# Kernel optimization log

Hardware: AMD Instinct MI355X
Metric: run time of the kernel (lower is better)

The kernel has to match this reference:

```python
import jax, jax.numpy as jnp
import numpy as np

D = 1024      # total input features
R = 32        # number of ragged regions
RMAX = 32     # max region size (padding target)
HIDDEN = [128, 128]
H1, H2 = HIDDEN
B = 8192      # batch size


def _made_masks(r, rmax, hidden):
    """TFP AutoregressiveNetwork masks (left-to-right order, 'equal' hidden degrees,
    params=2, use_bias=False), zero-padded to rmax features."""
    order = np.arange(1, r + 1)
    degs = [order]
    for u in hidden:
        mn = min(int(degs[-1].min()), r - 1)
        degs.append(np.maximum(mn, np.ceil(np.arange(1, u + 1) * (r - 1) / float(u + 1)).astype(np.int64)))
    m1 = np.zeros((rmax, hidden[0]), bool)
    m1[:r] = degs[0][:, None] <= degs[1][None, :]
    m2 = degs[1][:, None] <= degs[2][None, :]
    mout = np.zeros((hidden[-1], rmax * 2), bool)
    out_deg = np.repeat(order, 2)  # output layout is feature-major: [feat, param]
    mout[:, :2 * r] = degs[-1][:, None] < out_deg[None, :]
    return m1, m2, mout


def setup_inputs() -> dict:
    rng = np.random.default_rng(0)
    perm = rng.permutation(D)
    sizes = rng.integers(8, RMAX + 1, size=R)
    idx = np.zeros((R, RMAX), np.int64)
    valid = np.zeros((R, RMAX), bool)
    M1 = np.zeros((R, RMAX, H1), bool)
    M2 = np.zeros((R, H1, H2), bool)
    Mout = np.zeros((R, H2, RMAX * 2), bool)
    pos = 0
    for i in range(R):
        s = int(sizes[i])
        idx[i, :s] = perm[pos:pos + s]
        pos += s
        valid[i, :s] = True
        M1[i], M2[i], Mout[i] = _made_masks(s, RMAX, HIDDEN)
    key = jax.random.key(0)
    k1, k2, k3, k4 = jax.random.split(key, 4)
    inputs = jax.random.normal(k1, (B, D), jnp.float32)
    W1 = jax.random.normal(k2, (R, RMAX, H1), jnp.float32) / np.float32(np.sqrt(RMAX))
    W2 = jax.random.normal(k3, (R, H1, H2), jnp.float32) / np.float32(np.sqrt(H1))
    Wout = jax.random.normal(k4, (R, H2, RMAX * 2), jnp.float32) / np.float32(np.sqrt(H2))
    return {"inputs": inputs, "W1": W1, "W2": W2, "Wout": Wout,
            "idx": jnp.asarray(idx), "valid": jnp.asarray(valid),
            "M1": jnp.asarray(M1), "M2": jnp.asarray(M2), "Mout": jnp.asarray(Mout)}


def reference(inputs, W1, W2, Wout, idx, valid, M1, M2, Mout):
    f = inputs.dtype
    v = valid.astype(f)                              # [R, RMAX]
    xg = jnp.take(inputs, idx, axis=1) * v           # [B, R, RMAX] ragged gather (padded)
    # MADE masked MLP (relu, no bias), batched over all regions at once
    h1 = jax.nn.relu(jnp.einsum('brd,rdh->brh', xg, W1 * M1.astype(f)))
    h2 = jax.nn.relu(jnp.einsum('brh,rhk->brk', h1, W2 * M2.astype(f)))
    out = jnp.einsum('brk,rko->bro', h2, Wout * Mout.astype(f))
    out = out.reshape(out.shape[0], out.shape[1], RMAX, 2)
    shift, log_s = out[..., 0], out[..., 1]
    # MAF inverse: u = (x - shift) * exp(-log_scale); logdet = -sum(log_scale)
    u = (xg - shift) * jnp.exp(-log_s)
    elem = -0.5 * u * u - 0.5 * jnp.log(2.0 * jnp.pi) - log_s
    ll = jnp.sum(elem * v, axis=-1)                  # [B, R]
    return ll[..., None]                             # [B, R, 1] as in tf.stack of expand_dims
```

## Files before the change

### kernel.cpp

```cpp
#include <hip/hip_runtime.h>
#include <math.h>


#define RR 32
#define DD 1024
#define HH 128
#define OO 64
#define TROWS 32
#define TILES_PER_BLOCK 16
#define BLOCKS_PER_R 16

#define SHP 136
#define SXG 40
#define SXF 38
#define SSC 132

typedef short bf16x8_t __attribute__((ext_vector_type(8)));
typedef float f32x4_t __attribute__((ext_vector_type(4)));
typedef unsigned short u16;
typedef unsigned int u32;

__device__ __forceinline__ u16 bf16_rne(float x) {
    u32 u = __float_as_uint(x);
    u += 0x7FFFu + ((u >> 16) & 1u);
    return (u16)(u >> 16);
}
__device__ __forceinline__ float bf16_tof(u16 h) {
    return __uint_as_float(((u32)h) << 16);
}
__device__ __forceinline__ u16 lo_trunc(float v, u16 h) {
    return (u16)(__float_as_uint(v - bf16_tof(h)) >> 16);
}
__device__ __forceinline__ u32 pack_split(float v) {
    u16 h = bf16_rne(v);
    return (u32)h | ((u32)lo_trunc(v, h) << 16);
}
__device__ __forceinline__ void unpack8(const u32* p, bf16x8_t& hi, bf16x8_t& lo) {
    uint4 a = *reinterpret_cast<const uint4*>(p);
    uint4 b = *reinterpret_cast<const uint4*>(p + 4);
    union { u32 u[4]; bf16x8_t v; } H, L;
    H.u[0] = __builtin_amdgcn_perm(a.y, a.x, 0x05040100u);
    H.u[1] = __builtin_amdgcn_perm(a.w, a.z, 0x05040100u);
    H.u[2] = __builtin_amdgcn_perm(b.y, b.x, 0x05040100u);
    H.u[3] = __builtin_amdgcn_perm(b.w, b.z, 0x05040100u);
    L.u[0] = __builtin_amdgcn_perm(a.y, a.x, 0x07060302u);
    L.u[1] = __builtin_amdgcn_perm(a.w, a.z, 0x07060302u);
    L.u[2] = __builtin_amdgcn_perm(b.y, b.x, 0x07060302u);
    L.u[3] = __builtin_amdgcn_perm(b.w, b.z, 0x07060302u);
    hi = H.v; lo = L.v;
}
__device__ __forceinline__ f32x4_t mfma16(bf16x8_t a, bf16x8_t b, f32x4_t c) {
    return __builtin_amdgcn_mfma_f32_16x16x32_bf16(a, b, c, 0, 0, 0);
}

__device__ __forceinline__ void stage_block(const float* __restrict__ W,
                                            const int* __restrict__ M,
                                            int ldc, int c0, int K, u32* dst, int sd,
                                            int tid)
{
    const int kb = tid >> 3;
    const int cb = tid & 7;
    if (kb * 4 >= K) return;
    const int k0 = kb * 4;
    float e[4][4];
#pragma unroll
    for (int i = 0; i < 4; ++i) {
        const int o = ((k0 + i) * ldc + c0 + 4 * cb) >> 2;
        float4 w = ((const float4*)W)[o];
        int4   m = ((const int4*)M)[o];
        e[i][0] = m.x ? w.x : 0.f; e[i][1] = m.y ? w.y : 0.f;
        e[i][2] = m.z ? w.z : 0.f; e[i][3] = m.w ? w.w : 0.f;
    }
#pragma unroll
    for (int j = 0; j < 4; ++j) {
        uint4 p;
        p.x = pack_split(e[0][j]); p.y = pack_split(e[1][j]);
        p.z = pack_split(e[2][j]); p.w = pack_split(e[3][j]);
        *(uint4*)&dst[(4 * cb + j) * sd + k0] = p;
    }
}

__global__ __launch_bounds__(256, 2)
void made_flow_r9(const float* __restrict__ inputs,
                  const float* __restrict__ W1,
                  const float* __restrict__ W2,
                  const float* __restrict__ Wout,
                  const int* __restrict__ idx,
                  const int* __restrict__ valid,
                  const int* __restrict__ M1,
                  const int* __restrict__ M2,
                  const int* __restrict__ Mout,
                  float* __restrict__ out)
{
    __shared__ __align__(16) char regA[TROWS * SHP * 2 * 2];
    __shared__ __align__(16) char regB[TROWS * SHP * 2 * 2];
    __shared__ __align__(16) u16  xgh[2][TROWS * SXG];
    __shared__ __align__(16) u16  xgl[2][TROWS * SXG];
    __shared__ __align__(16) float xgf[2][TROWS * SXF];
    __shared__ __align__(16) float red_all[TILES_PER_BLOCK][TROWS][4];
    __shared__ int   idx_s[RR];
    __shared__ float v_s[RR];

    u16* const h1h = (u16*)regA;
    u16* const h1l = h1h + TROWS * SHP;
    u32* const scr = (u32*)regA;
    u16* const h2h = (u16*)regB;
    u16* const h2l = h2h + TROWS * SHP;

    const int tid  = threadIdx.x;
    const int r    = blockIdx.x / BLOCKS_PER_R;
    const int rb   = blockIdx.x % BLOCKS_PER_R;
    const int lane = tid & 63;
    const int wave = tid >> 6;
    const int q    = lane >> 4;
    const int l16  = lane & 15;

    if (tid < RR) {
        idx_s[tid] = idx[r * RR + tid];
        v_s[tid]   = valid[r * RR + tid] ? 1.f : 0.f;
    }

    bf16x8_t a1h[2], a1l[2];
    bf16x8_t a2h[2][4], a2l[2][4];
    bf16x8_t aoh[4],    aol[4];
    {
        const float* W1r = W1 + r * RR * HH;   const int* M1r = M1 + r * RR * HH;
        const float* W2r = W2 + r * HH * HH;   const int* M2r = M2 + r * HH * HH;
        const float* Wor = Wout + r * HH * OO; const int* Mor = Mout + r * HH * OO;
        for (int c = 0; c < 4; ++c) {
            __syncthreads();
            stage_block(W2r, M2r, HH, 32 * c, HH, scr, SSC, tid);
            __syncthreads();
            if (wave == c) {
#pragma unroll
                for (int mi = 0; mi < 2; ++mi)
#pragma unroll
                    for (int ks = 0; ks < 4; ++ks)
                        unpack8(&scr[(16 * mi + l16) * SSC + ks * 32 + q * 8],
                                a2h[mi][ks], a2l[mi][ks]);
            }
        }
        for (int c = 0; c < 2; ++c) {
            __syncthreads();
            stage_block(Wor, Mor, OO, 32 * c, HH, scr, SSC, tid);
            __syncthreads();
            if ((wave >> 1) == c) {
                const int nl = wave & 1;
#pragma unroll
                for (int ks = 0; ks < 4; ++ks)
                    unpack8(&scr[(16 * nl + l16) * SSC + ks * 32 + q * 8],
                            aoh[ks], aol[ks]);
            }
        }
        for (int c = 0; c < 4; ++c) {
            __syncthreads();
            stage_block(W1r, M1r, HH, 32 * c, RR, scr, SSC, tid);
            __syncthreads();
            if (wave == c) {
#pragma unroll
                for (int mi = 0; mi < 2; ++mi)
                    unpack8(&scr[(16 * mi + l16) * SSC + q * 8], a1h[mi], a1l[mi]);
            }
        }
    }
    __syncthreads();

    const f32x4_t zero4 = {0.f, 0.f, 0.f, 0.f};
    const int grow = tid >> 3, gg = tid & 7;

    {
        const int base = (rb * TILES_PER_BLOCK * TROWS + grow) * DD;
        float gx[4];
#pragma unroll
        for (int u = 0; u < 4; ++u)
            gx[u] = inputs[base + idx_s[4 * gg + u]] * v_s[4 * gg + u];
        ushort4 gh, gl;
        gh.x = bf16_rne(gx[0]); gl.x = lo_trunc(gx[0], gh.x);
        gh.y = bf16_rne(gx[1]); gl.y = lo_trunc(gx[1], gh.y);
        gh.z = bf16_rne(gx[2]); gl.z = lo_trunc(gx[2], gh.z);
        gh.w = bf16_rne(gx[3]); gl.w = lo_trunc(gx[3], gh.w);
        *(ushort4*)&xgh[0][grow * SXG + 4 * gg] = gh;
        *(ushort4*)&xgl[0][grow * SXG + 4 * gg] = gl;
        *(float2*)&xgf[0][grow * SXF + 4 * gg]     = make_float2(gx[0], gx[1]);
        *(float2*)&xgf[0][grow * SXF + 4 * gg + 2] = make_float2(gx[2], gx[3]);
    }
    __syncthreads();

    {
        bf16x8_t bh[2], bl[2];
#pragma unroll
        for (int ni = 0; ni < 2; ++ni) {
            bh[ni] = *(const bf16x8_t*)&xgh[0][(16 * ni + l16) * SXG + q * 8];
            bl[ni] = *(const bf16x8_t*)&xgl[0][(16 * ni + l16) * SXG + q * 8];
        }
#pragma unroll
        for (int mi = 0; mi < 2; ++mi)
#pragma unroll
            for (int ni = 0; ni < 2; ++ni) {
                f32x4_t a = zero4;
                a = mfma16(a1h[mi], bh[ni], a);
                a = mfma16(a1l[mi], bh[ni], a);
                a = mfma16(a1h[mi], bl[ni], a);
                ushort4 vh, vl;
                float v0 = fmaxf(a[0], 0.f), v1 = fmaxf(a[1], 0.f);
                float v2 = fmaxf(a[2], 0.f), v3 = fmaxf(a[3], 0.f);
                vh.x = bf16_rne(v0); vl.x = lo_trunc(v0, vh.x);
                vh.y = bf16_rne(v1); vl.y = lo_trunc(v1, vh.y);
                vh.z = bf16_rne(v2); vl.z = lo_trunc(v2, vh.z);
                vh.w = bf16_rne(v3); vl.w = lo_trunc(v3, vh.w);
                const int o = (16 * ni + l16) * SHP + 32 * wave + 16 * mi + 4 * q;
                *(ushort4*)&h1h[o] = vh;
                *(ushort4*)&h1l[o] = vl;
            }
    }

    for (int t = 0; t < TILES_PER_BLOCK; ++t) {
        const int row0 = (rb * TILES_PER_BLOCK + t) * TROWS;
        __syncthreads();

        float gx[4];
        const bool dg = (t + 1 < TILES_PER_BLOCK);
        if (dg) {
            const int base = (row0 + TROWS + grow) * DD;
#pragma unroll
            for (int u = 0; u < 4; ++u)
                gx[u] = inputs[base + idx_s[4 * gg + u]] * v_s[4 * gg + u];
        }
        {
            f32x4_t acc[2][2] = {{zero4, zero4}, {zero4, zero4}};
#pragma unroll
            for (int ks = 0; ks < 4; ++ks) {
#pragma unroll
                for (int ni = 0; ni < 2; ++ni) {
                    bf16x8_t bh = *(const bf16x8_t*)&h1h[(16 * ni + l16) * SHP + ks * 32 + q * 8];
                    bf16x8_t bl = *(const bf16x8_t*)&h1l[(16 * ni + l16) * SHP + ks * 32 + q * 8];
#pragma unroll
                    for (int mi = 0; mi < 2; ++mi) {
                        f32x4_t a = acc[mi][ni];
                        a = mfma16(a2h[mi][ks], bh, a);
                        a = mfma16(a2l[mi][ks], bh, a);
                        a = mfma16(a2h[mi][ks], bl, a);
                        acc[mi][ni] = a;
                    }
                }
            }
            if (dg) {
                const int b = (t + 1) & 1;
                ushort4 gh, gl;
                gh.x = bf16_rne(gx[0]); gl.x = lo_trunc(gx[0], gh.x);
                gh.y = bf16_rne(gx[1]); gl.y = lo_trunc(gx[1], gh.y);
                gh.z = bf16_rne(gx[2]); gl.z = lo_trunc(gx[2], gh.z);
                gh.w = bf16_rne(gx[3]); gl.w = lo_trunc(gx[3], gh.w);
                *(ushort4*)&xgh[b][grow * SXG + 4 * gg] = gh;
                *(ushort4*)&xgl[b][grow * SXG + 4 * gg] = gl;
                *(float2*)&xgf[b][grow * SXF + 4 * gg]     = make_float2(gx[0], gx[1]);
                *(float2*)&xgf[b][grow * SXF + 4 * gg + 2] = make_float2(gx[2], gx[3]);
            }
#pragma unroll
            for (int mi = 0; mi < 2; ++mi)
#pragma unroll
                for (int ni = 0; ni < 2; ++ni) {
                    ushort4 vh, vl;
                    float v0 = fmaxf(acc[mi][ni][0], 0.f), v1 = fmaxf(acc[mi][ni][1], 0.f);
                    float v2 = fmaxf(acc[mi][ni][2], 0.f), v3 = fmaxf(acc[mi][ni][3], 0.f);
                    vh.x = bf16_rne(v0); vl.x = lo_trunc(v0, vh.x);
                    vh.y = bf16_rne(v1); vl.y = lo_trunc(v1, vh.y);
                    vh.z = bf16_rne(v2); vl.z = lo_trunc(v2, vh.z);
                    vh.w = bf16_rne(v3); vl.w = lo_trunc(v3, vh.w);
                    const int o = (16 * ni + l16) * SHP + 32 * wave + 16 * mi + 4 * q;
                    *(ushort4*)&h2h[o] = vh;
                    *(ushort4*)&h2l[o] = vl;
                }
        }
        __syncthreads();

        f32x4_t acc3[2] = {zero4, zero4};
#pragma unroll
        for (int ks = 0; ks < 4; ++ks) {
#pragma unroll
            for (int ni = 0; ni < 2; ++ni) {
                bf16x8_t bh = *(const bf16x8_t*)&h2h[(16 * ni + l16) * SHP + ks * 32 + q * 8];
                bf16x8_t bl = *(const bf16x8_t*)&h2l[(16 * ni + l16) * SHP + ks * 32 + q * 8];
                f32x4_t a = acc3[ni];
                a = mfma16(aoh[ks], bh, a);
                a = mfma16(aol[ks], bh, a);
                a = mfma16(aoh[ks], bl, a);
                acc3[ni] = a;
            }
        }

        if (dg) {
            const int b = (t + 1) & 1;
            bf16x8_t bh[2], bl[2];
#pragma unroll
            for (int ni = 0; ni < 2; ++ni) {
                bh[ni] = *(const bf16x8_t*)&xgh[b][(16 * ni + l16) * SXG + q * 8];
                bl[ni] = *(const bf16x8_t*)&xgl[b][(16 * ni + l16) * SXG + q * 8];
            }
#pragma unroll
            for (int mi = 0; mi < 2; ++mi)
#pragma unroll
                for (int ni = 0; ni < 2; ++ni) {
                    f32x4_t a = zero4;
                    a = mfma16(a1h[mi], bh[ni], a);
                    a = mfma16(a1l[mi], bh[ni], a);
                    a = mfma16(a1h[mi], bl[ni], a);
                    ushort4 vh, vl;
                    float v0 = fmaxf(a[0], 0.f), v1 = fmaxf(a[1], 0.f);
                    float v2 = fmaxf(a[2], 0.f), v3 = fmaxf(a[3], 0.f);
                    vh.x = bf16_rne(v0); vl.x = lo_trunc(v0, vh.x);
                    vh.y = bf16_rne(v1); vl.y = lo_trunc(v1, vh.y);
                    vh.z = bf16_rne(v2); vl.z = lo_trunc(v2, vh.z);
                    vh.w = bf16_rne(v3); vl.w = lo_trunc(v3, vh.w);
                    const int o = (16 * ni + l16) * SHP + 32 * wave + 16 * mi + 4 * q;
                    *(ushort4*)&h1h[o] = vh;
                    *(ushort4*)&h1l[o] = vl;
                }
        }

        {
            const int j0 = 8 * wave + 2 * q;
            const float vj0 = v_s[j0], vj1 = v_s[j0 + 1];
            float p[2];
#pragma unroll
            for (int ni = 0; ni < 2; ++ni) {
                const int row = 16 * ni + l16;
                float2 xv = *(const float2*)&xgf[t & 1][row * SXF + j0];
                const float u0 = (xv.x - acc3[ni][0]) * __expf(-acc3[ni][1]);
                const float u1 = (xv.y - acc3[ni][2]) * __expf(-acc3[ni][3]);
                p[ni] = (-0.5f * u0 * u0 - 0.91893853320467266954f - acc3[ni][1]) * vj0
                      + (-0.5f * u1 * u1 - 0.91893853320467266954f - acc3[ni][3]) * vj1;
            }
#pragma unroll
            for (int ni = 0; ni < 2; ++ni) {
                p[ni] += __shfl_xor(p[ni], 16, 64);
                p[ni] += __shfl_xor(p[ni], 32, 64);
            }
            if (q == 0) {
#pragma unroll
                for (int ni = 0; ni < 2; ++ni)
                    red_all[t][16 * ni + l16][wave] = p[ni];
            }
        }
    }

    __syncthreads();
#pragma unroll
    for (int rep = 0; rep < 2; ++rep) {
        const int f   = tid + rep * 256;
        const int tt  = f >> 5;
        const int row = f & 31;
        float4 rv = *(const float4*)&red_all[tt][row][0];
        out[((rb * TILES_PER_BLOCK + tt) * TROWS + row) * RR + r] =
            rv.x + rv.y + rv.z + rv.w;
    }
}

extern "C" void kernel_launch(void* const* d_in, const int* in_sizes, int n_in,
                              void* d_out, int out_size, void* d_ws, size_t ws_size,
                              hipStream_t stream)
{
    const float* inputs = (const float*)d_in[0];
    const float* W1     = (const float*)d_in[1];
    const float* W2     = (const float*)d_in[2];
    const float* Wout   = (const float*)d_in[3];
    const int*   idx    = (const int*)d_in[4];
    const int*   valid  = (const int*)d_in[5];
    const int*   M1     = (const int*)d_in[6];
    const int*   M2     = (const int*)d_in[7];
    const int*   Mout   = (const int*)d_in[8];
    float*       out    = (float*)d_out;

    hipLaunchKernelGGL(made_flow_r9, dim3(RR * BLOCKS_PER_R), dim3(256), 0, stream,
                       inputs, W1, W2, Wout, idx, valid, M1, M2, Mout, out);
}
```

Before: 142.3 us.

## Double wavefronts per block, splitting MFMA tiles across eight waves

Raises the block from 256 to 512 threads. Each of the eight waves now holds half the register-resident weight fragments for W1, W2 and Wout and computes half the MFMA tiles per batch tile. Weight staging uses two scratch regions in parallel, one per half of the block, and the gather loads two elements per thread instead of four. The goal is more waves in flight to hide latency and less register pressure per wave. The cost is more threads contending at each barrier and a tighter launch bound of 4 blocks per unit.

```diff
diff --git a/kernel.cpp b/kernel.cpp
--- a/kernel.cpp
+++ b/kernel.cpp
@@ -80,17 +80,31 @@
     }
 }
 
-__global__ __launch_bounds__(256, 2)
-void made_flow_r9(const float* __restrict__ inputs,
-                  const float* __restrict__ W1,
-                  const float* __restrict__ W2,
-                  const float* __restrict__ Wout,
-                  const int* __restrict__ idx,
-                  const int* __restrict__ valid,
-                  const int* __restrict__ M1,
-                  const int* __restrict__ M2,
-                  const int* __restrict__ Mout,
-                  float* __restrict__ out)
+__device__ __forceinline__ void relu_pack_store(u16* __restrict__ h, u16* __restrict__ l,
+                                                int o, f32x4_t a)
+{
+    float v0 = fmaxf(a[0], 0.f), v1 = fmaxf(a[1], 0.f);
+    float v2 = fmaxf(a[2], 0.f), v3 = fmaxf(a[3], 0.f);
+    ushort4 vh, vl;
+    vh.x = bf16_rne(v0); vl.x = lo_trunc(v0, vh.x);
+    vh.y = bf16_rne(v1); vl.y = lo_trunc(v1, vh.y);
+    vh.z = bf16_rne(v2); vl.z = lo_trunc(v2, vh.z);
+    vh.w = bf16_rne(v3); vl.w = lo_trunc(v3, vh.w);
+    *(ushort4*)&h[o] = vh;
+    *(ushort4*)&l[o] = vl;
+}
+
+__global__ __launch_bounds__(512, 4)
+void made_flow_r10(const float* __restrict__ inputs,
+                   const float* __restrict__ W1,
+                   const float* __restrict__ W2,
+                   const float* __restrict__ Wout,
+                   const int* __restrict__ idx,
+                   const int* __restrict__ valid,
+                   const int* __restrict__ M1,
+                   const int* __restrict__ M2,
+                   const int* __restrict__ Mout,
+                   float* __restrict__ out)
 {
     __shared__ __align__(16) char regA[TROWS * SHP * 2 * 2];
     __shared__ __align__(16) char regB[TROWS * SHP * 2 * 2];
@@ -103,7 +117,8 @@
 
     u16* const h1h = (u16*)regA;
     u16* const h1l = h1h + TROWS * SHP;
-    u32* const scr = (u32*)regA;
+    u32* const scr  = (u32*)regA;
+    u32* const scr2 = (u32*)regB;
     u16* const h2h = (u16*)regB;
     u16* const h2l = h2h + TROWS * SHP;
 
@@ -114,75 +129,72 @@
     const int wave = tid >> 6;
     const int q    = lane >> 4;
     const int l16  = lane & 15;
+    const int wm3  = wave & 3;
+    const int ni3  = wave >> 2;
 
     if (tid < RR) {
         idx_s[tid] = idx[r * RR + tid];
         v_s[tid]   = valid[r * RR + tid] ? 1.f : 0.f;
     }
 
-    bf16x8_t a1h[2], a1l[2];
-    bf16x8_t a2h[2][4], a2l[2][4];
-    bf16x8_t aoh[4],    aol[4];
+    bf16x8_t a1h, a1l;
+    bf16x8_t a2h[4], a2l[4];
+    bf16x8_t aoh[4], aol[4];
     {
         const float* W1r = W1 + r * RR * HH;   const int* M1r = M1 + r * RR * HH;
         const float* W2r = W2 + r * HH * HH;   const int* M2r = M2 + r * HH * HH;
         const float* Wor = Wout + r * HH * OO; const int* Mor = Mout + r * HH * OO;
-        for (int c = 0; c < 4; ++c) {
-            __syncthreads();
-            stage_block(W2r, M2r, HH, 32 * c, HH, scr, SSC, tid);
-            __syncthreads();
-            if (wave == c) {
-#pragma unroll
-                for (int mi = 0; mi < 2; ++mi)
-#pragma unroll
-                    for (int ks = 0; ks < 4; ++ks)
-                        unpack8(&scr[(16 * mi + l16) * SSC + ks * 32 + q * 8],
-                                a2h[mi][ks], a2l[mi][ks]);
-            }
-        }
-        for (int c = 0; c < 2; ++c) {
-            __syncthreads();
-            stage_block(Wor, Mor, OO, 32 * c, HH, scr, SSC, tid);
-            __syncthreads();
-            if ((wave >> 1) == c) {
-                const int nl = wave & 1;
+        const int c = wave >> 1, h = wave & 1;
+        for (int i = 0; i < 2; ++i) {
+            __syncthreads();
+            if (tid < 256) stage_block(W2r, M2r, HH, 32 * (2 * i),     HH, scr,  SSC, tid);
+            else           stage_block(W2r, M2r, HH, 32 * (2 * i + 1), HH, scr2, SSC, tid - 256);
+            __syncthreads();
+            if (c == 2 * i) {
 #pragma unroll
                 for (int ks = 0; ks < 4; ++ks)
-                    unpack8(&scr[(16 * nl + l16) * SSC + ks * 32 + q * 8],
-                            aoh[ks], aol[ks]);
-            }
-        }
-        for (int c = 0; c < 4; ++c) {
-            __syncthreads();
-            stage_block(W1r, M1r, HH, 32 * c, RR, scr, SSC, tid);
-            __syncthreads();
-            if (wave == c) {
-#pragma unroll
-                for (int mi = 0; mi < 2; ++mi)
-                    unpack8(&scr[(16 * mi + l16) * SSC + q * 8], a1h[mi], a1l[mi]);
-            }
+                    unpack8(&scr[(16 * h + l16) * SSC + ks * 32 + q * 8], a2h[ks], a2l[ks]);
+            } else if (c == 2 * i + 1) {
+#pragma unroll
+                for (int ks = 0; ks < 4; ++ks)
+                    unpack8(&scr2[(16 * h + l16) * SSC + ks * 32 + q * 8], a2h[ks], a2l[ks]);
+            }
+        }
+        {
+            __syncthreads();
+            if (tid < 256) stage_block(Wor, Mor, OO, 0,  HH, scr,  SSC, tid);
+            else           stage_block(Wor, Mor, OO, 32, HH, scr2, SSC, tid - 256);
+            __syncthreads();
+            const u32* s = (wm3 >> 1) ? scr2 : scr;
+#pragma unroll
+            for (int ks = 0; ks < 4; ++ks)
+                unpack8(&s[(16 * (wm3 & 1) + l16) * SSC + ks * 32 + q * 8], aoh[ks], aol[ks]);
+        }
+        for (int i = 0; i < 2; ++i) {
+            __syncthreads();
+            if (tid < 256) stage_block(W1r, M1r, HH, 32 * (2 * i),     RR, scr,  SSC, tid);
+            else           stage_block(W1r, M1r, HH, 32 * (2 * i + 1), RR, scr2, SSC, tid - 256);
+            __syncthreads();
+            if (c == 2 * i)          unpack8(&scr [(16 * h + l16) * SSC + q * 8], a1h, a1l);
+            else if (c == 2 * i + 1) unpack8(&scr2[(16 * h + l16) * SSC + q * 8], a1h, a1l);
         }
     }
     __syncthreads();
 
     const f32x4_t zero4 = {0.f, 0.f, 0.f, 0.f};
-    const int grow = tid >> 3, gg = tid & 7;
+    const int grow = tid >> 4;
+    const int gg   = tid & 15;
 
     {
         const int base = (rb * TILES_PER_BLOCK * TROWS + grow) * DD;
-        float gx[4];
-#pragma unroll
-        for (int u = 0; u < 4; ++u)
-            gx[u] = inputs[base + idx_s[4 * gg + u]] * v_s[4 * gg + u];
-        ushort4 gh, gl;
-        gh.x = bf16_rne(gx[0]); gl.x = lo_trunc(gx[0], gh.x);
-        gh.y = bf16_rne(gx[1]); gl.y = lo_trunc(gx[1], gh.y);
-        gh.z = bf16_rne(gx[2]); gl.z = lo_trunc(gx[2], gh.z);
-        gh.w = bf16_rne(gx[3]); gl.w = lo_trunc(gx[3], gh.w);
-        *(ushort4*)&xgh[0][grow * SXG + 4 * gg] = gh;
-        *(ushort4*)&xgl[0][grow * SXG + 4 * gg] = gl;
-        *(float2*)&xgf[0][grow * SXF + 4 * gg]     = make_float2(gx[0], gx[1]);
-        *(float2*)&xgf[0][grow * SXF + 4 * gg + 2] = make_float2(gx[2], gx[3]);
+        float gx0 = inputs[base + idx_s[2 * gg]]     * v_s[2 * gg];
+        float gx1 = inputs[base + idx_s[2 * gg + 1]] * v_s[2 * gg + 1];
+        ushort2 gh, gl;
+        gh.x = bf16_rne(gx0); gl.x = lo_trunc(gx0, gh.x);
+        gh.y = bf16_rne(gx1); gl.y = lo_trunc(gx1, gh.y);
+        *(ushort2*)&xgh[0][grow * SXG + 2 * gg] = gh;
+        *(ushort2*)&xgl[0][grow * SXG + 2 * gg] = gl;
+        *(float2*)&xgf[0][grow * SXF + 2 * gg] = make_float2(gx0, gx1);
     }
     __syncthreads();
 
@@ -194,99 +206,64 @@
             bl[ni] = *(const bf16x8_t*)&xgl[0][(16 * ni + l16) * SXG + q * 8];
         }
 #pragma unroll
-        for (int mi = 0; mi < 2; ++mi)
-#pragma unroll
-            for (int ni = 0; ni < 2; ++ni) {
-                f32x4_t a = zero4;
-                a = mfma16(a1h[mi], bh[ni], a);
-                a = mfma16(a1l[mi], bh[ni], a);
-                a = mfma16(a1h[mi], bl[ni], a);
-                ushort4 vh, vl;
-                float v0 = fmaxf(a[0], 0.f), v1 = fmaxf(a[1], 0.f);
-                float v2 = fmaxf(a[2], 0.f), v3 = fmaxf(a[3], 0.f);
-                vh.x = bf16_rne(v0); vl.x = lo_trunc(v0, vh.x);
-                vh.y = bf16_rne(v1); vl.y = lo_trunc(v1, vh.y);
-                vh.z = bf16_rne(v2); vl.z = lo_trunc(v2, vh.z);
-                vh.w = bf16_rne(v3); vl.w = lo_trunc(v3, vh.w);
-                const int o = (16 * ni + l16) * SHP + 32 * wave + 16 * mi + 4 * q;
-                *(ushort4*)&h1h[o] = vh;
-                *(ushort4*)&h1l[o] = vl;
-            }
+        for (int ni = 0; ni < 2; ++ni) {
+            f32x4_t a = zero4;
+            a = mfma16(a1h, bh[ni], a);
+            a = mfma16(a1l, bh[ni], a);
+            a = mfma16(a1h, bl[ni], a);
+            relu_pack_store(h1h, h1l, (16 * ni + l16) * SHP + 16 * wave + 4 * q, a);
+        }
     }
 
     for (int t = 0; t < TILES_PER_BLOCK; ++t) {
         const int row0 = (rb * TILES_PER_BLOCK + t) * TROWS;
         __syncthreads();
 
-        float gx[4];
+        float gx0, gx1;
         const bool dg = (t + 1 < TILES_PER_BLOCK);
         if (dg) {
             const int base = (row0 + TROWS + grow) * DD;
-#pragma unroll
-            for (int u = 0; u < 4; ++u)
-                gx[u] = inputs[base + idx_s[4 * gg + u]] * v_s[4 * gg + u];
+            gx0 = inputs[base + idx_s[2 * gg]]     * v_s[2 * gg];
+            gx1 = inputs[base + idx_s[2 * gg + 1]] * v_s[2 * gg + 1];
         }
         {
-            f32x4_t acc[2][2] = {{zero4, zero4}, {zero4, zero4}};
+            f32x4_t acc[2] = {zero4, zero4};
 #pragma unroll
             for (int ks = 0; ks < 4; ++ks) {
 #pragma unroll
                 for (int ni = 0; ni < 2; ++ni) {
                     bf16x8_t bh = *(const bf16x8_t*)&h1h[(16 * ni + l16) * SHP + ks * 32 + q * 8];
                     bf16x8_t bl = *(const bf16x8_t*)&h1l[(16 * ni + l16) * SHP + ks * 32 + q * 8];
-#pragma unroll
-                    for (int mi = 0; mi < 2; ++mi) {
-                        f32x4_t a = acc[mi][ni];
-                        a = mfma16(a2h[mi][ks], bh, a);
-                        a = mfma16(a2l[mi][ks], bh, a);
-                        a = mfma16(a2h[mi][ks], bl, a);
-                        acc[mi][ni] = a;
-                    }
+                    f32x4_t a = acc[ni];
+                    a = mfma16(a2h[ks], bh, a);
+                    a = mfma16(a2l[ks], bh, a);
+                    a = mfma16(a2h[ks], bl, a);
+                    acc[ni] = a;
                 }
             }
             if (dg) {
                 const int b = (t + 1) & 1;
-                ushort4 gh, gl;
-                gh.x = bf16_rne(gx[0]); gl.x = lo_trunc(gx[0], gh.x);
-                gh.y = bf16_rne(gx[1]); gl.y = lo_trunc(gx[1], gh.y);
-                gh.z = bf16_rne(gx[2]); gl.z = lo_trunc(gx[2], gh.z);
-                gh.w = bf16_rne(gx[3]); gl.w = lo_trunc(gx[3], gh.w);
-                *(ushort4*)&xgh[b][grow * SXG + 4 * gg] = gh;
-                *(ushort4*)&xgl[b][grow * SXG + 4 * gg] = gl;
-                *(float2*)&xgf[b][grow * SXF + 4 * gg]     = make_float2(gx[0], gx[1]);
-                *(float2*)&xgf[b][grow * SXF + 4 * gg + 2] = make_float2(gx[2], gx[3]);
-            }
-#pragma unroll
-            for (int mi = 0; mi < 2; ++mi)
-#pragma unroll
-                for (int ni = 0; ni < 2; ++ni) {
-                    ushort4 vh, vl;
-                    float v0 = fmaxf(acc[mi][ni][0], 0.f), v1 = fmaxf(acc[mi][ni][1], 0.f);
-                    float v2 = fmaxf(acc[mi][ni][2], 0.f), v3 = fmaxf(acc[mi][ni][3], 0.f);
-                    vh.x = bf16_rne(v0); vl.x = lo_trunc(v0, vh.x);
-                    vh.y = bf16_rne(v1); vl.y = lo_trunc(v1, vh.y);
-                    vh.z = bf16_rne(v2); vl.z = lo_trunc(v2, vh.z);
-                    vh.w = bf16_rne(v3); vl.w = lo_trunc(v3, vh.w);
-                    const int o = (16 * ni + l16) * SHP + 32 * wave + 16 * mi + 4 * q;
-                    *(ushort4*)&h2h[o] = vh;
-                    *(ushort4*)&h2l[o] = vl;
-                }
+                ushort2 gh, gl;
+                gh.x = bf16_rne(gx0); gl.x = lo_trunc(gx0, gh.x);
+                gh.y = bf16_rne(gx1); gl.y = lo_trunc(gx1, gh.y);
+                *(ushort2*)&xgh[b][grow * SXG + 2 * gg] = gh;
+                *(ushort2*)&xgl[b][grow * SXG + 2 * gg] = gl;
+                *(float2*)&xgf[b][grow * SXF + 2 * gg] = make_float2(gx0, gx1);
+            }
+#pragma unroll
+            for (int ni = 0; ni < 2; ++ni)
+                relu_pack_store(h2h, h2l, (16 * ni + l16) * SHP + 16 * wave + 4 * q, acc[ni]);
         }
         __syncthreads();
 
-        f32x4_t acc3[2] = {zero4, zero4};
+        f32x4_t acc3 = zero4;
 #pragma unroll
         for (int ks = 0; ks < 4; ++ks) {
-#pragma unroll
-            for (int ni = 0; ni < 2; ++ni) {
-                bf16x8_t bh = *(const bf16x8_t*)&h2h[(16 * ni + l16) * SHP + ks * 32 + q * 8];
-                bf16x8_t bl = *(const bf16x8_t*)&h2l[(16 * ni + l16) * SHP + ks * 32 + q * 8];
-                f32x4_t a = acc3[ni];
-                a = mfma16(aoh[ks], bh, a);
-                a = mfma16(aol[ks], bh, a);
-                a = mfma16(aoh[ks], bl, a);
-                acc3[ni] = a;
-            }
+            bf16x8_t bh = *(const bf16x8_t*)&h2h[(16 * ni3 + l16) * SHP + ks * 32 + q * 8];
+            bf16x8_t bl = *(const bf16x8_t*)&h2l[(16 * ni3 + l16) * SHP + ks * 32 + q * 8];
+            acc3 = mfma16(aoh[ks], bh, acc3);
+            acc3 = mfma16(aol[ks], bh, acc3);
+            acc3 = mfma16(aoh[ks], bl, acc3);
         }
 
         if (dg) {
@@ -298,58 +275,34 @@
                 bl[ni] = *(const bf16x8_t*)&xgl[b][(16 * ni + l16) * SXG + q * 8];
             }
 #pragma unroll
-            for (int mi = 0; mi < 2; ++mi)
-#pragma unroll
-                for (int ni = 0; ni < 2; ++ni) {
-                    f32x4_t a = zero4;
-                    a = mfma16(a1h[mi], bh[ni], a);
-                    a = mfma16(a1l[mi], bh[ni], a);
-                    a = mfma16(a1h[mi], bl[ni], a);
-                    ushort4 vh, vl;
-                    float v0 = fmaxf(a[0], 0.f), v1 = fmaxf(a[1], 0.f);
-                    float v2 = fmaxf(a[2], 0.f), v3 = fmaxf(a[3], 0.f);
-                    vh.x = bf16_rne(v0); vl.x = lo_trunc(v0, vh.x);
-                    vh.y = bf16_rne(v1); vl.y = lo_trunc(v1, vh.y);
-                    vh.z = bf16_rne(v2); vl.z = lo_trunc(v2, vh.z);
-                    vh.w = bf16_rne(v3); vl.w = lo_trunc(v3, vh.w);
-                    const int o = (16 * ni + l16) * SHP + 32 * wave + 16 * mi + 4 * q;
-                    *(ushort4*)&h1h[o] = vh;
-                    *(ushort4*)&h1l[o] = vl;
-                }
+            for (int ni = 0; ni < 2; ++ni) {
+                f32x4_t a = zero4;
+                a = mfma16(a1h, bh[ni], a);
+                a = mfma16(a1l, bh[ni], a);
+                a = mfma16(a1h, bl[ni], a);
+                relu_pack_store(h1h, h1l, (16 * ni + l16) * SHP + 16 * wave + 4 * q, a);
+            }
         }
 
         {
-            const int j0 = 8 * wave + 2 * q;
+            const int j0 = 8 * wm3 + 2 * q;
             const float vj0 = v_s[j0], vj1 = v_s[j0 + 1];
-            float p[2];
-#pragma unroll
-            for (int ni = 0; ni < 2; ++ni) {
-                const int row = 16 * ni + l16;
-                float2 xv = *(const float2*)&xgf[t & 1][row * SXF + j0];
-                const float u0 = (xv.x - acc3[ni][0]) * __expf(-acc3[ni][1]);
-                const float u1 = (xv.y - acc3[ni][2]) * __expf(-acc3[ni][3]);
-                p[ni] = (-0.5f * u0 * u0 - 0.91893853320467266954f - acc3[ni][1]) * vj0
-                      + (-0.5f * u1 * u1 - 0.91893853320467266954f - acc3[ni][3]) * vj1;
-            }
-#pragma unroll
-            for (int ni = 0; ni < 2; ++ni) {
-                p[ni] += __shfl_xor(p[ni], 16, 64);
-                p[ni] += __shfl_xor(p[ni], 32, 64);
-            }
-            if (q == 0) {
-#pragma unroll
-                for (int ni = 0; ni < 2; ++ni)
-                    red_all[t][16 * ni + l16][wave] = p[ni];
-            }
+            const int row = 16 * ni3 + l16;
+            float2 xv = *(const float2*)&xgf[t & 1][row * SXF + j0];
+            const float u0 = (xv.x - acc3[0]) * __expf(-acc3[1]);
+            const float u1 = (xv.y - acc3[2]) * __expf(-acc3[3]);
+            float p = (-0.5f * u0 * u0 - 0.91893853320467266954f - acc3[1]) * vj0
+                    + (-0.5f * u1 * u1 - 0.91893853320467266954f - acc3[3]) * vj1;
+            p += __shfl_xor(p, 16, 64);
+            p += __shfl_xor(p, 32, 64);
+            if (q == 0) red_all[t][row][wm3] = p;
         }
     }
 
     __syncthreads();
-#pragma unroll
-    for (int rep = 0; rep < 2; ++rep) {
-        const int f   = tid + rep * 256;
-        const int tt  = f >> 5;
-        const int row = f & 31;
+    {
+        const int tt  = tid >> 5;
+        const int row = tid & 31;
         float4 rv = *(const float4*)&red_all[tt][row][0];
         out[((rb * TILES_PER_BLOCK + tt) * TROWS + row) * RR + r] =
             rv.x + rv.y + rv.z + rv.w;
@@ -371,6 +324,6 @@
     const int*   Mout   = (const int*)d_in[8];
     float*       out    = (float*)d_out;
 
-    hipLaunchKernelGGL(made_flow_r9, dim3(RR * BLOCKS_PER_R), dim3(256), 0, stream,
+    hipLaunchKernelGGL(made_flow_r10, dim3(RR * BLOCKS_PER_R), dim3(512), 0, stream,
                        inputs, W1, W2, Wout, idx, valid, M1, M2, Mout, out);
 }
```

Measured after the change: 137.8 us. -3.2%, faster.
